# Kernel optimization log

Measured on AMD Instinct MI355X. Metric: run time of the kernel, lower is better.

## Reference

```python
import jax, jax.numpy as jnp
import numpy as np

N = 15000        # nodes
E = 240000       # edges (avg degree 16)
IN_DIM = 100
HID = 128
N_ETYPES = 13
N_STEPS = 6
N_GRAPHS = 64
N_CLASSES = 10


def setup_inputs() -> dict:
    key = jax.random.key(0)
    ks = jax.random.split(key, 12)
    feat = jax.random.normal(ks[0], (N, IN_DIM), dtype=jnp.float32)
    src = jax.random.randint(ks[1], (E,), 0, N, dtype=jnp.int32)
    dst = jax.random.randint(ks[2], (E,), 0, N, dtype=jnp.int32)
    etypes = jax.random.randint(ks[3], (E,), 0, N_ETYPES, dtype=jnp.int32)
    graph_ids = jnp.sort(jax.random.randint(ks[4], (N,), 0, N_GRAPHS, dtype=jnp.int32))
    s = 1.0 / np.sqrt(HID)
    W_e = jax.random.normal(ks[5], (N_ETYPES, HID, HID), dtype=jnp.float32) * s
    b_e = jax.random.normal(ks[6], (N_ETYPES, HID), dtype=jnp.float32) * s
    W_ih = jax.random.normal(ks[7], (3 * HID, HID), dtype=jnp.float32) * s
    W_hh = jax.random.normal(ks[8], (3 * HID, HID), dtype=jnp.float32) * s
    b_ih = jax.random.normal(ks[9], (3 * HID,), dtype=jnp.float32) * s
    b_hh = jax.random.normal(ks[10], (3 * HID,), dtype=jnp.float32) * s
    W_cls = jax.random.normal(ks[11], (N_CLASSES, HID), dtype=jnp.float32) * s
    b_cls = jnp.zeros((N_CLASSES,), dtype=jnp.float32)
    return {"feat": feat, "src": src, "dst": dst, "etypes": etypes,
            "graph_ids": graph_ids, "W_e": W_e, "b_e": b_e,
            "W_ih": W_ih, "W_hh": W_hh, "b_ih": b_ih, "b_hh": b_hh,
            "W_cls": W_cls, "b_cls": b_cls}


def _ggnn_forward(feat, src, dst, etypes, graph_ids, W_e, b_e, W_ih, W_hh, b_ih, b_hh, W_cls, b_cls):
    # DGL GatedGraphConv: zero-pad input features up to out_feats
    h = jnp.pad(feat, ((0, 0), (0, HID - IN_DIM)))  # [N, HID]
    for _ in range(N_STEPS):
        # per-etype linear transform of all nodes: [T, N, HID]
        Wh = jnp.einsum('nd,tdh->tnh', h, W_e) + b_e[:, None, :]
        # per-edge message = linear[etype](h[src]) via gather; scatter-sum to dst
        msg = Wh[etypes, src]                                  # [E, HID]
        a = jax.ops.segment_sum(msg, dst, num_segments=N)      # [N, HID]
        # torch GRUCell update (gate order r, z, n)
        gi = a @ W_ih.T + b_ih
        gh = h @ W_hh.T + b_hh
        ir, iz, inn = jnp.split(gi, 3, axis=-1)
        hr, hz, hn = jnp.split(gh, 3, axis=-1)
        r = jax.nn.sigmoid(ir + hr)
        z = jax.nn.sigmoid(iz + hz)
        n = jnp.tanh(inn + r * hn)
        h = (1.0 - z) * n + z * h
    # dgl.sum_nodes: sum node states per graph in the batch
    hg = jax.ops.segment_sum(h, graph_ids, num_segments=N_GRAPHS)  # [G, HID]
    return hg @ W_cls.T + b_cls                                    # [G, N_CLASSES]


def reference(feat, src, dst, etypes, graph_ids, W_e, b_e, W_ih, W_hh, b_ih, b_hh, W_cls, b_cls):
    return _ggnn_forward(feat, src, dst, etypes, graph_ids, W_e, b_e, W_ih, W_hh, b_ih, b_hh, W_cls, b_cls)
```

## Files before the change

### kernel.cpp

```cpp
#include <hip/hip_runtime.h>
#include <math.h>

#define N_NODES 15000
#define NPAD    15104
#define E_EDGES 240000
#define IN_DIM  100
#define HID     128
#define N_ETYPES 13
#define N_STEPS  6
#define N_GRAPHS 64
#define N_CLASSES 10

typedef short v8bf __attribute__((ext_vector_type(8)));
typedef float v4f  __attribute__((ext_vector_type(4)));

union FragU { uint4 u; v8bf b; };

static __device__ __forceinline__ float bf2f(unsigned short u) {
    union { unsigned int i; float f; } x; x.i = ((unsigned int)u) << 16; return x.f;
}
static __device__ __forceinline__ unsigned short f2bf(float f) {
    union { float f; unsigned int i; } x; x.f = f;
    unsigned int u = x.i;
    u = (u + 0x7fff + ((u >> 16) & 1)) >> 16;
    return (unsigned short)u;
}
static __device__ __forceinline__ float sigm(float x) { return 1.f / (1.f + expf(-x)); }

__global__ __launch_bounds__(256) void k_zero(float* __restrict__ p, long n4) {
    long i = (long)blockIdx.x * 256 + threadIdx.x;
    if (i < n4) ((float4*)p)[i] = make_float4(0.f, 0.f, 0.f, 0.f);
}

__global__ __launch_bounds__(256) void k_init_h(const float* __restrict__ feat,
                                                float* __restrict__ h32,
                                                unsigned short* __restrict__ h_hi,
                                                unsigned short* __restrict__ h_lo) {
    int idx = blockIdx.x * 256 + threadIdx.x;
    if (idx >= NPAD * HID) return;
    int n = idx >> 7, c = idx & 127;
    float v = 0.f;
    if (n < N_NODES && c < IN_DIM) v = feat[n * IN_DIM + c];
    h32[idx] = v;
    unsigned short hi = f2bf(v);
    h_hi[idx] = hi;
    h_lo[idx] = f2bf(v - bf2f(hi));
}

__global__ __launch_bounds__(256) void k_prepW(
    const float* __restrict__ W_e, const float* __restrict__ W_ih, const float* __restrict__ W_hh,
    unsigned short* __restrict__ WeH, unsigned short* __restrict__ WeL,
    unsigned short* __restrict__ WihH, unsigned short* __restrict__ WihL,
    unsigned short* __restrict__ WhhH, unsigned short* __restrict__ WhhL)
{
    int f = blockIdx.x * 256 + threadIdx.x;
    const int NE = N_ETYPES * 2048;
    const int NG = 16 * 384;
    unsigned short th[8], tl[8];
    if (f < NE) {
        int t = f >> 11, r = f & 2047, kcsub = r >> 7, c = r & 127;
        #pragma unroll
        for (int j = 0; j < 8; ++j) {
            float w = W_e[(long)t * 16384 + (kcsub * 8 + j) * 128 + c];
            th[j] = f2bf(w); tl[j] = f2bf(w - bf2f(th[j]));
        }
        long off = (long)t * 16384 + ((kcsub << 7) + c) * 8;
        *(uint4*)(WeH + off) = *(uint4*)th;
        *(uint4*)(WeL + off) = *(uint4*)tl;
    } else if (f < NE + 2 * NG) {
        int f2 = f - NE;
        const float* srcp = (f2 < NG) ? W_ih : W_hh;
        unsigned short* dh = (f2 < NG) ? WihH : WhhH;
        unsigned short* dl = (f2 < NG) ? WihL : WhhL;
        int g = (f2 < NG) ? f2 : f2 - NG;
        int kcsub = g / 384, c = g - kcsub * 384;
        #pragma unroll
        for (int j = 0; j < 8; ++j) {
            float w = srcp[(long)c * 128 + kcsub * 8 + j];
            th[j] = f2bf(w); tl[j] = f2bf(w - bf2f(th[j]));
        }
        long off = ((long)kcsub * 384 + c) * 8;
        *(uint4*)(dh + off) = *(uint4*)th;
        *(uint4*)(dl + off) = *(uint4*)tl;
    }
}

__global__ __launch_bounds__(256) void k_count(const int* __restrict__ dst, int* __restrict__ deg) {
    int e = blockIdx.x * 256 + threadIdx.x;
    if (e < E_EDGES) atomicAdd(&deg[dst[e]], 1);
}

__global__ __launch_bounds__(1024) void k_scan(const int* __restrict__ deg,
                                               int* __restrict__ rowptr, int* __restrict__ cursor) {
    __shared__ int part[1024];
    int tid = threadIdx.x;
    const int CH = 15;
    int base = tid * CH;
    int local[CH]; int s = 0;
    #pragma unroll
    for (int i = 0; i < CH; ++i) {
        int d = (base + i < NPAD) ? deg[base + i] : 0;
        local[i] = s; s += d;
    }
    part[tid] = s; __syncthreads();
    for (int off = 1; off < 1024; off <<= 1) {
        int v = (tid >= off) ? part[tid - off] : 0;
        __syncthreads();
        part[tid] += v;
        __syncthreads();
    }
    int excl = (tid > 0) ? part[tid - 1] : 0;
    #pragma unroll
    for (int i = 0; i < CH; ++i)
        if (base + i < NPAD) { rowptr[base + i] = excl + local[i]; cursor[base + i] = excl + local[i]; }
    if (tid == 0) rowptr[NPAD] = part[1023];
}

__global__ __launch_bounds__(256) void k_fill(const int* __restrict__ src, const int* __restrict__ dst,
                                              const int* __restrict__ et, int* __restrict__ cursor,
                                              int* __restrict__ eidx) {
    int e = blockIdx.x * 256 + threadIdx.x;
    if (e >= E_EDGES) return;
    int d = dst[e];
    int pos = atomicAdd(&cursor[d], 1);
    eidx[pos] = et[e] * NPAD + src[e];
}

__global__ __launch_bounds__(512) void k_egemm(
    const unsigned short* __restrict__ Ahi, const unsigned short* __restrict__ Alo,
    const uint4* __restrict__ BH, const uint4* __restrict__ BL,
    const float* __restrict__ bias, unsigned short* __restrict__ C)
{
    __shared__ uint4 blds[2][2048];
    const int NW = 118 * N_ETYPES;
    const int q = NW / 8, r8 = NW % 8;
    int bid = blockIdx.x;
    int xcd = bid & 7, ii = bid >> 3;
    int lid = (xcd < r8 ? xcd * (q + 1) : r8 * (q + 1) + (xcd - r8) * q) + ii;
    int rg = lid / N_ETYPES, t = lid - rg * N_ETYPES;

    int tid = threadIdx.x;
    {
        const uint4* bh = BH + t * 2048;
        const uint4* bl = BL + t * 2048;
        #pragma unroll
        for (int it = 0; it < 4; ++it) {
            int f = it * 512 + tid;
            blds[0][f] = bh[f];
            blds[1][f] = bl[f];
        }
    }
    __syncthreads();

    int lane = tid & 63, w = tid >> 6;
    int r0 = rg * 128 + w * 16;
    int l15 = lane & 15, lsub = lane >> 4;

    FragU ah[4], al[4];
    const char* Ahb = (const char*)Ahi;
    const char* Alb = (const char*)Alo;
    #pragma unroll
    for (int kc = 0; kc < 4; ++kc) {
        long boff = (long)(r0 + l15) * 256 + kc * 64 + lsub * 16;
        ah[kc].u = *(const uint4*)(Ahb + boff);
        al[kc].u = *(const uint4*)(Alb + boff);
    }

    v4f acc[8];
    #pragma unroll
    for (int c8 = 0; c8 < 8; ++c8) acc[c8] = (v4f)(0.f);

    #pragma unroll
    for (int kc = 0; kc < 4; ++kc)
        #pragma unroll
        for (int c8 = 0; c8 < 8; ++c8) {
            int bi = (kc * 4 + lsub) * 128 + c8 * 16 + l15;
            FragU bhf, blf; bhf.u = blds[0][bi]; blf.u = blds[1][bi];
            acc[c8] = __builtin_amdgcn_mfma_f32_16x16x32_bf16(ah[kc].b, bhf.b, acc[c8], 0, 0, 0);
            acc[c8] = __builtin_amdgcn_mfma_f32_16x16x32_bf16(al[kc].b, bhf.b, acc[c8], 0, 0, 0);
            acc[c8] = __builtin_amdgcn_mfma_f32_16x16x32_bf16(ah[kc].b, blf.b, acc[c8], 0, 0, 0);
        }

    const float* bs = bias + t * 128;
    unsigned short* Ct = C + (long)t * NPAD * 128;
    int rbase = r0 + lsub * 4;
    #pragma unroll
    for (int c8 = 0; c8 < 8; ++c8) {
        int col = c8 * 16 + l15;
        float bv = bs[col];
        #pragma unroll
        for (int i = 0; i < 4; ++i) {
            int row = rbase + i;
            if (row < N_NODES) Ct[(long)row * 128 + col] = f2bf(acc[c8][i] + bv);
        }
    }
}

__global__ __launch_bounds__(512) void k_ggemm(
    const unsigned short* __restrict__ A0h, const unsigned short* __restrict__ A0l,
    const unsigned short* __restrict__ A1h, const unsigned short* __restrict__ A1l,
    const uint4* __restrict__ B0H, const uint4* __restrict__ B0L,
    const uint4* __restrict__ B1H, const uint4* __restrict__ B1L,
    const float* __restrict__ bias0, const float* __restrict__ bias1,
    unsigned short* __restrict__ C0, unsigned short* __restrict__ C1)
{
    __shared__ uint4 blds[2][2048];
    int z = blockIdx.z;
    const unsigned short* Ahi = z ? A1h : A0h;
    const unsigned short* Alo = z ? A1l : A0l;
    const uint4* BH = z ? B1H : B0H;
    const uint4* BL = z ? B1L : B0L;
    const float* bias = z ? bias1 : bias0;
    unsigned short* C = z ? C1 : C0;
    int j0 = blockIdx.y * 128;

    int tid = threadIdx.x;
    {
        #pragma unroll
        for (int it = 0; it < 4; ++it) {
            int f = it * 512 + tid;
            int kcsub = f >> 7, c = f & 127;
            int gi = kcsub * 384 + j0 + c;
            blds[0][f] = BH[gi];
            blds[1][f] = BL[gi];
        }
    }
    __syncthreads();

    int lane = tid & 63, w = tid >> 6;
    int r0 = blockIdx.x * 128 + w * 16;
    int l15 = lane & 15, lsub = lane >> 4;

    FragU ah[4], al[4];
    const char* Ahb = (const char*)Ahi;
    const char* Alb = (const char*)Alo;
    #pragma unroll
    for (int kc = 0; kc < 4; ++kc) {
        long boff = (long)(r0 + l15) * 256 + kc * 64 + lsub * 16;
        ah[kc].u = *(const uint4*)(Ahb + boff);
        al[kc].u = *(const uint4*)(Alb + boff);
    }

    v4f acc[8];
    #pragma unroll
    for (int c8 = 0; c8 < 8; ++c8) acc[c8] = (v4f)(0.f);

    #pragma unroll
    for (int kc = 0; kc < 4; ++kc)
        #pragma unroll
        for (int c8 = 0; c8 < 8; ++c8) {
            int bi = (kc * 4 + lsub) * 128 + c8 * 16 + l15;
            FragU bhf, blf; bhf.u = blds[0][bi]; blf.u = blds[1][bi];
            acc[c8] = __builtin_amdgcn_mfma_f32_16x16x32_bf16(ah[kc].b, bhf.b, acc[c8], 0, 0, 0);
            acc[c8] = __builtin_amdgcn_mfma_f32_16x16x32_bf16(al[kc].b, bhf.b, acc[c8], 0, 0, 0);
            acc[c8] = __builtin_amdgcn_mfma_f32_16x16x32_bf16(ah[kc].b, blf.b, acc[c8], 0, 0, 0);
        }

    int rbase = r0 + lsub * 4;
    #pragma unroll
    for (int c8 = 0; c8 < 8; ++c8) {
        int col = j0 + c8 * 16 + l15;
        float bv = bias[col];
        #pragma unroll
        for (int i = 0; i < 4; ++i) {
            int row = rbase + i;
            if (row < N_NODES) C[(long)row * 384 + col] = f2bf(acc[c8][i] + bv);
        }
    }
}

__global__ __launch_bounds__(256) void k_agg(
    const int* __restrict__ rowptr, const int* __restrict__ eidx,
    const unsigned int* __restrict__ Wh,
    unsigned int* __restrict__ a_hi, unsigned int* __restrict__ a_lo)
{
    int d = blockIdx.x * 4 + (threadIdx.x >> 6);
    if (d >= NPAD) return;
    int lane = threadIdx.x & 63;
    int s = rowptr[d], e = rowptr[d + 1];
    float a0 = 0.f, a1 = 0.f, b0 = 0.f, b1 = 0.f;
    int i = s;
    for (; i + 3 < e; i += 4) {
        int w0 = eidx[i], w1 = eidx[i + 1], w2 = eidx[i + 2], w3 = eidx[i + 3];
        unsigned int v0 = Wh[(long)w0 * 64 + lane];
        unsigned int v1 = Wh[(long)w1 * 64 + lane];
        unsigned int v2 = Wh[(long)w2 * 64 + lane];
        unsigned int v3 = Wh[(long)w3 * 64 + lane];
        a0 += bf2f((unsigned short)(v0 & 0xffff)) + bf2f((unsigned short)(v2 & 0xffff));
        a1 += bf2f((unsigned short)(v0 >> 16))    + bf2f((unsigned short)(v2 >> 16));
        b0 += bf2f((unsigned short)(v1 & 0xffff)) + bf2f((unsigned short)(v3 & 0xffff));
        b1 += bf2f((unsigned short)(v1 >> 16))    + bf2f((unsigned short)(v3 >> 16));
    }
    for (; i < e; ++i) {
        unsigned int v0 = Wh[(long)eidx[i] * 64 + lane];
        a0 += bf2f((unsigned short)(v0 & 0xffff));
        a1 += bf2f((unsigned short)(v0 >> 16));
    }
    a0 += b0; a1 += b1;
    unsigned short h0 = f2bf(a0), h1 = f2bf(a1);
    unsigned short l0 = f2bf(a0 - bf2f(h0)), l1 = f2bf(a1 - bf2f(h1));
    a_hi[(long)d * 64 + lane] = (unsigned int)h0 | ((unsigned int)h1 << 16);
    a_lo[(long)d * 64 + lane] = (unsigned int)l0 | ((unsigned int)l1 << 16);
}

__global__ __launch_bounds__(256) void k_gates(
    const unsigned short* __restrict__ GI, const unsigned short* __restrict__ GH,
    float* __restrict__ h32,
    unsigned int* __restrict__ h_hi, unsigned int* __restrict__ h_lo)
{
    int idx = blockIdx.x * 256 + threadIdx.x;
    if (idx >= N_NODES * 64) return;
    int n = idx >> 6, c2 = idx & 63;
    const unsigned int* gi = (const unsigned int*)(GI + (long)n * 384);
    const unsigned int* gh = (const unsigned int*)(GH + (long)n * 384);
    unsigned int uir = gi[c2], uiz = gi[c2 + 64], uin = gi[c2 + 128];
    unsigned int uhr = gh[c2], uhz = gh[c2 + 64], uhn = gh[c2 + 128];
    float2 ho = ((float2*)h32)[idx];
    float hv[2];
    #pragma unroll
    for (int p = 0; p < 2; ++p) {
        int sh = p * 16;
        float ir = bf2f((unsigned short)(uir >> sh)), iz = bf2f((unsigned short)(uiz >> sh)),
              inn = bf2f((unsigned short)(uin >> sh));
        float hr = bf2f((unsigned short)(uhr >> sh)), hz = bf2f((unsigned short)(uhz >> sh)),
              hn = bf2f((unsigned short)(uhn >> sh));
        float rr = sigm(ir + hr);
        float zg = sigm(iz + hz);
        float ng = tanhf(inn + rr * hn);
        float hov = p ? ho.y : ho.x;
        hv[p] = (1.f - zg) * ng + zg * hov;
    }
    ((float2*)h32)[idx] = make_float2(hv[0], hv[1]);
    unsigned short hi0 = f2bf(hv[0]), hi1 = f2bf(hv[1]);
    h_hi[idx] = (unsigned int)hi0 | ((unsigned int)hi1 << 16);
    unsigned short lo0 = f2bf(hv[0] - bf2f(hi0)), lo1 = f2bf(hv[1] - bf2f(hi1));
    h_lo[idx] = (unsigned int)lo0 | ((unsigned int)lo1 << 16);
}

__global__ __launch_bounds__(256) void k_pool(const float* __restrict__ h32,
                                              const int* __restrict__ gid,
                                              float* __restrict__ hg) {
    int idx = blockIdx.x * 256 + threadIdx.x;
    if (idx >= N_NODES * HID) return;
    int n = idx >> 7, c = idx & 127;
    atomicAdd(&hg[gid[n] * HID + c], h32[idx]);
}

__global__ __launch_bounds__(640) void k_cls(const float* __restrict__ hg,
                                             const float* __restrict__ Wc,
                                             const float* __restrict__ bc,
                                             float* __restrict__ out) {
    int tid = threadIdx.x;
    if (tid >= N_GRAPHS * N_CLASSES) return;
    int g = tid / N_CLASSES, c = tid - g * N_CLASSES;
    float s = bc[c];
    for (int k = 0; k < HID; ++k) s = fmaf(hg[g * HID + k], Wc[c * HID + k], s);
    out[tid] = s;
}

extern "C" void kernel_launch(void* const* d_in, const int* in_sizes, int n_in,
                              void* d_out, int out_size, void* d_ws, size_t ws_size,
                              hipStream_t stream) {
    const float* feat  = (const float*)d_in[0];
    const int*   src   = (const int*)d_in[1];
    const int*   dst   = (const int*)d_in[2];
    const int*   et    = (const int*)d_in[3];
    const int*   gid   = (const int*)d_in[4];
    const float* W_e   = (const float*)d_in[5];
    const float* b_e   = (const float*)d_in[6];
    const float* W_ih  = (const float*)d_in[7];
    const float* W_hh  = (const float*)d_in[8];
    const float* b_ih  = (const float*)d_in[9];
    const float* b_hh  = (const float*)d_in[10];
    const float* W_cls = (const float*)d_in[11];
    const float* b_cls = (const float*)d_in[12];
    float* out = (float*)d_out;

    char* p = (char*)d_ws;
    auto alloc = [&](size_t bytes) { char* r = p; p += (bytes + 255) & ~(size_t)255; return r; };
    float*          h32  = (float*)alloc((size_t)NPAD * 128 * 4);
    unsigned short* h_hi = (unsigned short*)alloc((size_t)NPAD * 128 * 2);
    unsigned short* h_lo = (unsigned short*)alloc((size_t)NPAD * 128 * 2);
    unsigned short* a_hi = (unsigned short*)alloc((size_t)NPAD * 128 * 2);
    unsigned short* a_lo = (unsigned short*)alloc((size_t)NPAD * 128 * 2);
    unsigned short* Wh   = (unsigned short*)alloc((size_t)N_ETYPES * NPAD * 128 * 2);
    unsigned short* GI   = (unsigned short*)alloc((size_t)NPAD * 384 * 2);
    unsigned short* GH   = (unsigned short*)alloc((size_t)NPAD * 384 * 2);
    unsigned short* WeH  = (unsigned short*)alloc((size_t)N_ETYPES * 16384 * 2);
    unsigned short* WeL  = (unsigned short*)alloc((size_t)N_ETYPES * 16384 * 2);
    unsigned short* WihH = (unsigned short*)alloc((size_t)16 * 384 * 8 * 2);
    unsigned short* WihL = (unsigned short*)alloc((size_t)16 * 384 * 8 * 2);
    unsigned short* WhhH = (unsigned short*)alloc((size_t)16 * 384 * 8 * 2);
    unsigned short* WhhL = (unsigned short*)alloc((size_t)16 * 384 * 8 * 2);
    int* deg    = (int*)alloc((size_t)NPAD * 4);
    int* rowptr = (int*)alloc((size_t)(NPAD + 1) * 4);
    int* cursor = (int*)alloc((size_t)NPAD * 4);
    int* eidx   = (int*)alloc((size_t)E_EDGES * 4);
    float* hg   = (float*)alloc((size_t)N_GRAPHS * HID * 4);

    k_init_h<<<(NPAD * HID + 255) / 256, 256, 0, stream>>>(feat, h32, h_hi, h_lo);
    k_prepW<<<(N_ETYPES * 2048 + 2 * 16 * 384 + 255) / 256, 256, 0, stream>>>(
        W_e, W_ih, W_hh, WeH, WeL, WihH, WihL, WhhH, WhhL);
    k_zero<<<(NPAD / 4 + 255) / 256, 256, 0, stream>>>((float*)deg, NPAD / 4);
    k_count<<<(E_EDGES + 255) / 256, 256, 0, stream>>>(dst, deg);
    k_scan<<<1, 1024, 0, stream>>>(deg, rowptr, cursor);
    k_fill<<<(E_EDGES + 255) / 256, 256, 0, stream>>>(src, dst, et, cursor, eidx);

    dim3 gG(118, 3, 2);
    for (int step = 0; step < N_STEPS; ++step) {
        k_egemm<<<118 * N_ETYPES, 512, 0, stream>>>(
            h_hi, h_lo, (const uint4*)WeH, (const uint4*)WeL, b_e, Wh);
        k_agg<<<NPAD / 4, 256, 0, stream>>>(rowptr, eidx, (const unsigned int*)Wh,
                                            (unsigned int*)a_hi, (unsigned int*)a_lo);
        k_ggemm<<<gG, 512, 0, stream>>>(
            a_hi, a_lo, h_hi, h_lo,
            (const uint4*)WihH, (const uint4*)WihL, (const uint4*)WhhH, (const uint4*)WhhL,
            b_ih, b_hh, GI, GH);
        k_gates<<<(N_NODES * 64 + 255) / 256, 256, 0, stream>>>(
            GI, GH, h32, (unsigned int*)h_hi, (unsigned int*)h_lo);
    }

    k_zero<<<(N_GRAPHS * HID / 4 + 255) / 256, 256, 0, stream>>>(hg, N_GRAPHS * HID / 4);
    k_pool<<<(N_NODES * HID + 255) / 256, 256, 0, stream>>>(h32, gid, hg);
    k_cls<<<1, 640, 0, stream>>>(hg, W_cls, b_cls, out);
}
```

Before: 582.6 us.

## Fuse GRU input/hidden GEMMs with gate update into one kernel

Replaces the separate k_ggemm (which wrote the GI and GH gate pre-activations to global memory in bf16) and k_gates kernels with one k_gru kernel. Each wave computes all three gate tiles for both the input and hidden projections in registers, then applies the sigmoid/tanh update and writes h32, h_hi and h_lo directly. This removes the GI/GH global round trip and one launch per step. In exchange, weights are read straight from global memory or cache instead of LDS, the grid is smaller (236 blocks), and h_hi/h_lo are updated in place, which depends on the block-level barrier placed after the fragment loads.

```diff
diff --git a/kernel.cpp b/kernel.cpp
--- a/kernel.cpp
+++ b/kernel.cpp
@@ -192,79 +192,6 @@
         for (int i = 0; i < 4; ++i) {
             int row = rbase + i;
             if (row < N_NODES) Ct[(long)row * 128 + col] = f2bf(acc[c8][i] + bv);
-        }
-    }
-}
-
-__global__ __launch_bounds__(512) void k_ggemm(
-    const unsigned short* __restrict__ A0h, const unsigned short* __restrict__ A0l,
-    const unsigned short* __restrict__ A1h, const unsigned short* __restrict__ A1l,
-    const uint4* __restrict__ B0H, const uint4* __restrict__ B0L,
-    const uint4* __restrict__ B1H, const uint4* __restrict__ B1L,
-    const float* __restrict__ bias0, const float* __restrict__ bias1,
-    unsigned short* __restrict__ C0, unsigned short* __restrict__ C1)
-{
-    __shared__ uint4 blds[2][2048];
-    int z = blockIdx.z;
-    const unsigned short* Ahi = z ? A1h : A0h;
-    const unsigned short* Alo = z ? A1l : A0l;
-    const uint4* BH = z ? B1H : B0H;
-    const uint4* BL = z ? B1L : B0L;
-    const float* bias = z ? bias1 : bias0;
-    unsigned short* C = z ? C1 : C0;
-    int j0 = blockIdx.y * 128;
-
-    int tid = threadIdx.x;
-    {
-        #pragma unroll
-        for (int it = 0; it < 4; ++it) {
-            int f = it * 512 + tid;
-            int kcsub = f >> 7, c = f & 127;
-            int gi = kcsub * 384 + j0 + c;
-            blds[0][f] = BH[gi];
-            blds[1][f] = BL[gi];
-        }
-    }
-    __syncthreads();
-
-    int lane = tid & 63, w = tid >> 6;
-    int r0 = blockIdx.x * 128 + w * 16;
-    int l15 = lane & 15, lsub = lane >> 4;
-
-    FragU ah[4], al[4];
-    const char* Ahb = (const char*)Ahi;
-    const char* Alb = (const char*)Alo;
-    #pragma unroll
-    for (int kc = 0; kc < 4; ++kc) {
-        long boff = (long)(r0 + l15) * 256 + kc * 64 + lsub * 16;
-        ah[kc].u = *(const uint4*)(Ahb + boff);
-        al[kc].u = *(const uint4*)(Alb + boff);
-    }
-
-    v4f acc[8];
-    #pragma unroll
-    for (int c8 = 0; c8 < 8; ++c8) acc[c8] = (v4f)(0.f);
-
-    #pragma unroll
-    for (int kc = 0; kc < 4; ++kc)
-        #pragma unroll
-        for (int c8 = 0; c8 < 8; ++c8) {
-            int bi = (kc * 4 + lsub) * 128 + c8 * 16 + l15;
-            FragU bhf, blf; bhf.u = blds[0][bi]; blf.u = blds[1][bi];
-            acc[c8] = __builtin_amdgcn_mfma_f32_16x16x32_bf16(ah[kc].b, bhf.b, acc[c8], 0, 0, 0);
-            acc[c8] = __builtin_amdgcn_mfma_f32_16x16x32_bf16(al[kc].b, bhf.b, acc[c8], 0, 0, 0);
-            acc[c8] = __builtin_amdgcn_mfma_f32_16x16x32_bf16(ah[kc].b, blf.b, acc[c8], 0, 0, 0);
-        }
-
-    int rbase = r0 + lsub * 4;
-    #pragma unroll
-    for (int c8 = 0; c8 < 8; ++c8) {
-        int col = j0 + c8 * 16 + l15;
-        float bv = bias[col];
-        #pragma unroll
-        for (int i = 0; i < 4; ++i) {
-            int row = rbase + i;
-            if (row < N_NODES) C[(long)row * 384 + col] = f2bf(acc[c8][i] + bv);
         }
     }
 }
@@ -303,38 +230,80 @@
     a_lo[(long)d * 64 + lane] = (unsigned int)l0 | ((unsigned int)l1 << 16);
 }
 
-__global__ __launch_bounds__(256) void k_gates(
-    const unsigned short* __restrict__ GI, const unsigned short* __restrict__ GH,
+__global__ __launch_bounds__(512) void k_gru(
+    const unsigned short* __restrict__ a_hi, const unsigned short* __restrict__ a_lo,
+    const uint4* __restrict__ WihH, const uint4* __restrict__ WihL,
+    const uint4* __restrict__ WhhH, const uint4* __restrict__ WhhL,
+    const float* __restrict__ b_ih, const float* __restrict__ b_hh,
     float* __restrict__ h32,
-    unsigned int* __restrict__ h_hi, unsigned int* __restrict__ h_lo)
+    unsigned short* __restrict__ h_hi, unsigned short* __restrict__ h_lo)
 {
-    int idx = blockIdx.x * 256 + threadIdx.x;
-    if (idx >= N_NODES * 64) return;
-    int n = idx >> 6, c2 = idx & 63;
-    const unsigned int* gi = (const unsigned int*)(GI + (long)n * 384);
-    const unsigned int* gh = (const unsigned int*)(GH + (long)n * 384);
-    unsigned int uir = gi[c2], uiz = gi[c2 + 64], uin = gi[c2 + 128];
-    unsigned int uhr = gh[c2], uhz = gh[c2 + 64], uhn = gh[c2 + 128];
-    float2 ho = ((float2*)h32)[idx];
-    float hv[2];
-    #pragma unroll
-    for (int p = 0; p < 2; ++p) {
-        int sh = p * 16;
-        float ir = bf2f((unsigned short)(uir >> sh)), iz = bf2f((unsigned short)(uiz >> sh)),
-              inn = bf2f((unsigned short)(uin >> sh));
-        float hr = bf2f((unsigned short)(uhr >> sh)), hz = bf2f((unsigned short)(uhz >> sh)),
-              hn = bf2f((unsigned short)(uhn >> sh));
-        float rr = sigm(ir + hr);
-        float zg = sigm(iz + hz);
-        float ng = tanhf(inn + rr * hn);
-        float hov = p ? ho.y : ho.x;
-        hv[p] = (1.f - zg) * ng + zg * hov;
-    }
-    ((float2*)h32)[idx] = make_float2(hv[0], hv[1]);
-    unsigned short hi0 = f2bf(hv[0]), hi1 = f2bf(hv[1]);
-    h_hi[idx] = (unsigned int)hi0 | ((unsigned int)hi1 << 16);
-    unsigned short lo0 = f2bf(hv[0] - bf2f(hi0)), lo1 = f2bf(hv[1] - bf2f(hi1));
-    h_lo[idx] = (unsigned int)lo0 | ((unsigned int)lo1 << 16);
+    int tid = threadIdx.x, lane = tid & 63, w = tid >> 6;
+    int gw = blockIdx.x * 8 + w;
+    int rgp = gw >> 1, half = gw & 1;
+    int r0 = rgp * 16;
+    int l15 = lane & 15, lsub = lane >> 4;
+
+    FragU aa[2][4], hh[2][4];
+    {
+        const char* ahb = (const char*)a_hi;
+        const char* alb = (const char*)a_lo;
+        const char* hhb = (const char*)h_hi;
+        const char* hlb = (const char*)h_lo;
+        #pragma unroll
+        for (int kc = 0; kc < 4; ++kc) {
+            long boff = (long)(r0 + l15) * 256 + kc * 64 + lsub * 16;
+            aa[0][kc].u = *(const uint4*)(ahb + boff);
+            aa[1][kc].u = *(const uint4*)(alb + boff);
+            hh[0][kc].u = *(const uint4*)(hhb + boff);
+            hh[1][kc].u = *(const uint4*)(hlb + boff);
+        }
+    }
+    __syncthreads();
+
+    #pragma unroll
+    for (int u = 0; u < 4; ++u) {
+        int cg = half * 4 + u;
+        v4f accI[3], accH[3];
+        #pragma unroll
+        for (int g = 0; g < 3; ++g) { accI[g] = (v4f)(0.f); accH[g] = (v4f)(0.f); }
+
+        #pragma unroll
+        for (int kc = 0; kc < 4; ++kc)
+            #pragma unroll
+            for (int g = 0; g < 3; ++g) {
+                int bi = (kc * 4 + lsub) * 384 + g * 128 + cg * 16 + l15;
+                FragU wih_h, wih_l, whh_h, whh_l;
+                wih_h.u = WihH[bi]; wih_l.u = WihL[bi];
+                whh_h.u = WhhH[bi]; whh_l.u = WhhL[bi];
+                accI[g] = __builtin_amdgcn_mfma_f32_16x16x32_bf16(aa[0][kc].b, wih_h.b, accI[g], 0, 0, 0);
+                accI[g] = __builtin_amdgcn_mfma_f32_16x16x32_bf16(aa[1][kc].b, wih_h.b, accI[g], 0, 0, 0);
+                accI[g] = __builtin_amdgcn_mfma_f32_16x16x32_bf16(aa[0][kc].b, wih_l.b, accI[g], 0, 0, 0);
+                accH[g] = __builtin_amdgcn_mfma_f32_16x16x32_bf16(hh[0][kc].b, whh_h.b, accH[g], 0, 0, 0);
+                accH[g] = __builtin_amdgcn_mfma_f32_16x16x32_bf16(hh[1][kc].b, whh_h.b, accH[g], 0, 0, 0);
+                accH[g] = __builtin_amdgcn_mfma_f32_16x16x32_bf16(hh[0][kc].b, whh_l.b, accH[g], 0, 0, 0);
+            }
+
+        int c = cg * 16 + l15;
+        float bir = b_ih[c], biz = b_ih[c + 128], bin = b_ih[c + 256];
+        float bhr = b_hh[c], bhz = b_hh[c + 128], bhn = b_hh[c + 256];
+        #pragma unroll
+        for (int i = 0; i < 4; ++i) {
+            int row = r0 + lsub * 4 + i;
+            float ir = accI[0][i] + bir, iz = accI[1][i] + biz, inn = accI[2][i] + bin;
+            float hr = accH[0][i] + bhr, hz = accH[1][i] + bhz, hn = accH[2][i] + bhn;
+            float rr = sigm(ir + hr);
+            float zg = sigm(iz + hz);
+            float ng = tanhf(inn + rr * hn);
+            long off = (long)row * 128 + c;
+            float ho = h32[off];
+            float hv = (1.f - zg) * ng + zg * ho;
+            h32[off] = hv;
+            unsigned short hi_ = f2bf(hv);
+            h_hi[off] = hi_;
+            h_lo[off] = f2bf(hv - bf2f(hi_));
+        }
+    }
 }
 
 __global__ __launch_bounds__(256) void k_pool(const float* __restrict__ h32,
@@ -384,8 +353,6 @@
     unsigned short* a_hi = (unsigned short*)alloc((size_t)NPAD * 128 * 2);
     unsigned short* a_lo = (unsigned short*)alloc((size_t)NPAD * 128 * 2);
     unsigned short* Wh   = (unsigned short*)alloc((size_t)N_ETYPES * NPAD * 128 * 2);
-    unsigned short* GI   = (unsigned short*)alloc((size_t)NPAD * 384 * 2);
-    unsigned short* GH   = (unsigned short*)alloc((size_t)NPAD * 384 * 2);
     unsigned short* WeH  = (unsigned short*)alloc((size_t)N_ETYPES * 16384 * 2);
     unsigned short* WeL  = (unsigned short*)alloc((size_t)N_ETYPES * 16384 * 2);
     unsigned short* WihH = (unsigned short*)alloc((size_t)16 * 384 * 8 * 2);
@@ -406,18 +373,15 @@
     k_scan<<<1, 1024, 0, stream>>>(deg, rowptr, cursor);
     k_fill<<<(E_EDGES + 255) / 256, 256, 0, stream>>>(src, dst, et, cursor, eidx);
 
-    dim3 gG(118, 3, 2);
     for (int step = 0; step < N_STEPS; ++step) {
         k_egemm<<<118 * N_ETYPES, 512, 0, stream>>>(
             h_hi, h_lo, (const uint4*)WeH, (const uint4*)WeL, b_e, Wh);
         k_agg<<<NPAD / 4, 256, 0, stream>>>(rowptr, eidx, (const unsigned int*)Wh,
                                             (unsigned int*)a_hi, (unsigned int*)a_lo);
-        k_ggemm<<<gG, 512, 0, stream>>>(
-            a_hi, a_lo, h_hi, h_lo,
+        k_gru<<<236, 512, 0, stream>>>(
+            a_hi, a_lo,
             (const uint4*)WihH, (const uint4*)WihL, (const uint4*)WhhH, (const uint4*)WhhL,
-            b_ih, b_hh, GI, GH);
-        k_gates<<<(N_NODES * 64 + 255) / 256, 256, 0, stream>>>(
-            GI, GH, h32, (unsigned int*)h_hi, (unsigned int*)h_lo);
+            b_ih, b_hh, h32, h_hi, h_lo);
     }
 
     k_zero<<<(N_GRAPHS * HID / 4 + 255) / 256, 256, 0, stream>>>(hg, N_GRAPHS * HID / 4);
```

Result: slower. 626.4 us (+7.5%).
